# Kernel tuning notes

Measured on AMD Instinct MI355X. Metric: run time of the kernel, lower is better.

The kernel has to match this reference:

```python
import jax, jax.numpy as jnp
import numpy as np

B, N, C0, N0 = 2, 4096, 128, 10242
IN_CH = 19  # 16 class-label + 3 xyz channels of `original`
EPS = 1e-5


def setup_inputs() -> dict:
    key = jax.random.key(0)
    ks = jax.random.split(key, 8)
    original = jax.random.normal(ks[0], (B, IN_CH, N), dtype=jnp.float32)
    projected = jax.random.normal(ks[1], (B, C0, N0), dtype=jnp.float32)
    vertex = jax.random.normal(ks[2], (N0, 3), dtype=jnp.float32)
    near_idx = jax.random.randint(ks[3], (N0, 6), 1, N0)  # low=1 so threshold > 0
    W0 = jax.random.normal(ks[4], (128, IN_CH + C0), dtype=jnp.float32) * 0.02
    W1 = jax.random.normal(ks[5], (128, 128), dtype=jnp.float32) * 0.02
    W2 = jax.random.normal(ks[6], (128, 128), dtype=jnp.float32) * 0.02
    z = jnp.zeros((128,), jnp.float32)
    o = jnp.ones((128,), jnp.float32)
    return {
        'original': original, 'projected': projected, 'vertex': vertex,
        'near_idx': near_idx,
        'W0': W0, 'b0': z, 'g0': o, 'be0': z,
        'W1': W1, 'b1': z, 'g1': o, 'be1': z,
        'W2': W2, 'b2': z, 'g2': o, 'be2': z,
    }


def _sf_to_pc(proj_f, vertex, near_idx, xyz):
    # proj_f: [B, N0, C0] features per mesh vertex; xyz: [B, N, 3]
    r = jnp.sqrt(jnp.sum(vertex[0] ** 2))  # sphere radius of fractal mesh
    # spherical projection of xyz onto sphere radius r (same direction)
    pxyz = xyz * (r / jnp.linalg.norm(xyz, axis=-1, keepdims=True))  # [B,N,3]
    # threshold = dist(vertex[0], vertex[near_idx[0,0]]); compare squared dists
    t2 = jnp.sum((vertex[0] - vertex[near_idx[0, 0]]) ** 2)
    # squared distances via GEMM: |p|^2 = r^2 (on sphere)
    v2 = jnp.sum(vertex ** 2, axis=-1)  # [N0]
    d2 = r * r + v2[None, None, :] - 2.0 * jnp.einsum('bnd,md->bnm', pxyz, vertex)
    mask = d2 <= t2                              # [B,N,N0]
    has = jnp.any(mask, axis=-1)                 # [B,N]
    first = jnp.argmax(mask, axis=-1)            # first matching vertex (early-exit semantics)
    feat = jnp.take_along_axis(proj_f, first[..., None], axis=1)  # [B,N,C0]
    return jnp.where(has[..., None], feat, 0.0)


def _conv_bn_relu(x, W, b, g, be):
    # x: [B,N,Cin]; 1x1 Conv1d == per-point linear; BN over (B,N) per channel (train mode)
    y = jnp.einsum('bnc,oc->bno', x, W) + b
    mean = jnp.mean(y, axis=(0, 1))
    var = jnp.var(y, axis=(0, 1))
    y = g * (y - mean) * jax.lax.rsqrt(var + EPS) + be
    return jax.nn.relu(y)


def reference(original, projected, vertex, near_idx,
              W0, b0, g0, be0, W1, b1, g1, be1, W2, b2, g2, be2):
    orig = jnp.transpose(original, (0, 2, 1))    # [B,N,19]
    proj_f = jnp.transpose(projected, (0, 2, 1))  # [B,N0,C0]
    xyz = orig[:, :, :3]
    feat = _sf_to_pc(proj_f, vertex, near_idx, xyz)      # [B,N,C0]
    x = jnp.concatenate([orig, feat], axis=-1)           # [B,N,19+C0]
    x = _conv_bn_relu(x, W0, b0, g0, be0)
    x = _conv_bn_relu(x, W1, b1, g1, be1)
    x = _conv_bn_relu(x, W2, b2, g2, be2)
    return jnp.transpose(x, (0, 2, 1))  # [B,128,N]
```

## Files before the change

### kernel.cpp

```cpp
#include <hip/hip_runtime.h>

#define NPTS 4096
#define N0V  10242
#define EPSV 1e-5f
#define SLOTS 16

typedef unsigned short ushortT;
typedef __attribute__((ext_vector_type(8))) short short8;
typedef __attribute__((ext_vector_type(4))) float f32x4;

__device__ __forceinline__ float fmul(float a,float b){return __fmul_rn(a,b);}
__device__ __forceinline__ float fadd(float a,float b){return __fadd_rn(a,b);}
__device__ __forceinline__ float fsub(float a,float b){return __fsub_rn(a,b);}

__device__ __forceinline__ ushortT f2bf(float x){
  unsigned u = __float_as_uint(x);
  u = (u + 0x7fffu + ((u>>16)&1u)) >> 16;
  return (ushortT)u;
}
__device__ __forceinline__ float bf2f(ushortT u){
  return __uint_as_float(((unsigned)u) << 16);
}

template<int NS>
__device__ __forceinline__ void tile_mm(const ushortT* xa, const ushortT* wt, int wstr,
    int li, int hi, int rt, int colg, f32x4& acc)
{
  acc = (f32x4){0.f,0.f,0.f,0.f};
  const ushortT* wbp = wt + colg*wstr + hi*8;
  const ushortT* xap = xa + (rt*16 + li)*168 + hi*8;
  #pragma unroll
  for (int s=0;s<NS;s++){
    short8 bb = *(const short8*)(wbp + s*32);
    short8 a0 = *(const short8*)(xap + s*32);
    acc = __builtin_amdgcn_mfma_f32_16x16x32_bf16(a0, bb, acc, 0,0,0);
  }
}

__device__ __forceinline__ void tile_partials(const f32x4& acc, float* __restrict__ slotL,
                                              int blk, int lane, int colg)
{
  float s1=0.f, s2=0.f;
  #pragma unroll
  for (int r=0;r<4;r++){ s1 += acc[r]; s2 = fmaf(acc[r],acc[r],s2); }
  s1 += __shfl_xor(s1,16); s1 += __shfl_xor(s1,32);
  s2 += __shfl_xor(s2,16); s2 += __shfl_xor(s2,32);
  if (lane < 16){
    float* sl = slotL + (blk & (SLOTS-1))*256;
    atomicAdd(&sl[colg], s1);
    atomicAdd(&sl[128 + colg], s2);
  }
}

__device__ __forceinline__ void slot_stats(const float* __restrict__ slotL,
    const float* __restrict__ g, const float* __restrict__ be,
    float* red2, float* stS, float* stB, int t)
{
  if (t < 256){
    float v = 0.f;
    #pragma unroll
    for (int s=0;s<SLOTS;s++) v += slotL[s*256 + t];
    red2[t] = v;
  }
  __syncthreads();
  if (t < 128){
    float S = red2[t], Q = red2[128 + t];
    float mean = S * (1.0f/8192.0f);
    float var  = Q * (1.0f/8192.0f) - mean*mean;
    float inv  = 1.0f / __fsqrt_rn(var + EPSV);
    float sc = g[t]*inv;
    stS[t] = sc;
    stB[t] = be[t] - mean*sc;
  }
  __syncthreads();
}

__global__ __launch_bounds__(1024) void k_l0(
    const float* __restrict__ orig, const float* __restrict__ proj,
    const float* __restrict__ vertex, const int* __restrict__ nidx,
    const float* __restrict__ W0, const float* __restrict__ b0,
    float* __restrict__ slot0, float* __restrict__ slotZ,
    ushortT* __restrict__ y0)
{
  __shared__ __align__(16) ushortT wt[128*168];
  __shared__ __align__(16) ushortT xa[32*168];

  const int t    = threadIdx.x;
  const int blk  = blockIdx.x;
  const int lane = t & 63;
  const int w    = t >> 6;
  const int b    = blk >> 7;
  const int n0   = (blk & 127) * 32;
  const int li   = lane & 15;
  const int hi   = lane >> 4;
  const int rt   = w >> 3;
  const int colg = (w & 7)*16 + li;

  if (blk < 8) slotZ[blk*1024 + t] = 0.f;

  for (int u = t; u < 21504; u += 1024){
    int o = u/168, k = u - o*168;
    wt[u] = f2bf((k < 147) ? W0[o*147 + k] : 0.f);
  }

  {
    float v0x=vertex[0], v0y=vertex[1], v0z=vertex[2];
    float r  = __fsqrt_rn(fadd(fadd(fmul(v0x,v0x),fmul(v0y,v0y)),fmul(v0z,v0z)));
    float rr = fmul(r,r);
    int j0 = nidx[0];
    float ax=vertex[3*j0], ay=vertex[3*j0+1], az=vertex[3*j0+2];
    float dx=fsub(v0x,ax), dy=fsub(v0y,ay), dz=fsub(v0z,az);
    float t2 = fadd(fadd(fmul(dx,dx),fmul(dy,dy)),fmul(dz,dz));

    #pragma unroll
    for (int rr_i=0; rr_i<2; rr_i++){
      const int row = w*2 + rr_i;
      const int n = n0 + row;
      const float* ob = orig + (b*19)*NPTS + n;
      float x=ob[0], y=ob[NPTS], z=ob[2*NPTS];
      float nrm = __fsqrt_rn(fadd(fadd(fmul(x,x),fmul(y,y)),fmul(z,z)));
      float s = __fdiv_rn(r,nrm);
      float px=fmul(x,s), py=fmul(y,s), pz=fmul(z,s);

      int first=0, has=0;
      for (int c0=0; c0<N0V; c0+=256){
        int m0=min(c0+lane,N0V-1), m1=min(c0+lane+64,N0V-1),
            m2=min(c0+lane+128,N0V-1), m3=min(c0+lane+192,N0V-1);
        float a0x=vertex[3*m0],a0y=vertex[3*m0+1],a0z=vertex[3*m0+2];
        float a1x=vertex[3*m1],a1y=vertex[3*m1+1],a1z=vertex[3*m1+2];
        float a2x=vertex[3*m2],a2y=vertex[3*m2+1],a2z=vertex[3*m2+2];
        float a3x=vertex[3*m3],a3y=vertex[3*m3+1],a3z=vertex[3*m3+2];
        float v20=fadd(fadd(fmul(a0x,a0x),fmul(a0y,a0y)),fmul(a0z,a0z));
        float v21=fadd(fadd(fmul(a1x,a1x),fmul(a1y,a1y)),fmul(a1z,a1z));
        float v22=fadd(fadd(fmul(a2x,a2x),fmul(a2y,a2y)),fmul(a2z,a2z));
        float v23=fadd(fadd(fmul(a3x,a3x),fmul(a3y,a3y)),fmul(a3z,a3z));
        float d0=fadd(fadd(fmul(px,a0x),fmul(py,a0y)),fmul(pz,a0z));
        float d1=fadd(fadd(fmul(px,a1x),fmul(py,a1y)),fmul(pz,a1z));
        float d2=fadd(fadd(fmul(px,a2x),fmul(py,a2y)),fmul(pz,a2z));
        float d3=fadd(fadd(fmul(px,a3x),fmul(py,a3y)),fmul(pz,a3z));
        bool h0 = (c0+lane    <N0V) && (fsub(fadd(rr,v20),fmul(2.0f,d0)) <= t2);
        bool h1 = (c0+lane+64 <N0V) && (fsub(fadd(rr,v21),fmul(2.0f,d1)) <= t2);
        bool h2 = (c0+lane+128<N0V) && (fsub(fadd(rr,v22),fmul(2.0f,d2)) <= t2);
        bool h3 = (c0+lane+192<N0V) && (fsub(fadd(rr,v23),fmul(2.0f,d3)) <= t2);
        unsigned long long bal;
        if ((bal=__ballot(h0))){ first=c0     +__builtin_ctzll(bal); has=1; break; }
        if ((bal=__ballot(h1))){ first=c0+ 64+__builtin_ctzll(bal); has=1; break; }
        if ((bal=__ballot(h2))){ first=c0+128+__builtin_ctzll(bal); has=1; break; }
        if ((bal=__ballot(h3))){ first=c0+192+__builtin_ctzll(bal); has=1; break; }
      }

      ushortT* rowp = xa + row*168;
      const float* pb = proj + (long)b*128*N0V;
      #pragma unroll
      for (int k=0;k<3;k++){
        int idx = lane + k*64;
        if (idx < 168){
          float v;
          if (idx < 19)        v = orig[(b*19+idx)*NPTS + n];
          else if (idx < 147)  v = has ? pb[(long)(idx-19)*N0V + first] : 0.0f;
          else                 v = 0.0f;
          rowp[idx] = f2bf(v);
        }
      }
    }
  }
  __syncthreads();

  f32x4 acc;
  tile_mm<5>(xa, wt, 168, li, hi, rt, colg, acc);
  float bo = b0[colg];
  #pragma unroll
  for (int r=0;r<4;r++) acc[r] += bo;
  tile_partials(acc, slot0, blk, lane, colg);
  #pragma unroll
  for (int r=0;r<4;r++)
    y0[(long)(b*4096 + n0 + rt*16 + hi*4 + r)*128 + colg] = f2bf(acc[r]);
}

__global__ __launch_bounds__(1024) void k_lmid(
    const ushortT* __restrict__ yin, const float* __restrict__ slotPrev,
    const float* __restrict__ g, const float* __restrict__ be,
    const float* __restrict__ W, const float* __restrict__ bias,
    float* __restrict__ slotCur, ushortT* __restrict__ yout)
{
  __shared__ __align__(16) ushortT wt[128*136];
  __shared__ __align__(16) ushortT xa[32*168];
  __shared__ float red2[256];
  __shared__ float stS[128];
  __shared__ float stB[128];

  const int t    = threadIdx.x;
  const int blk  = blockIdx.x;
  const int lane = t & 63;
  const int w    = t >> 6;
  const int n0   = blk * 32;
  const int li   = lane & 15;
  const int hi   = lane >> 4;
  const int rt   = w >> 3;
  const int colg = (w & 7)*16 + li;

  for (int u = t; u < 17408; u += 1024){
    int o = u/136, k = u - o*136;
    wt[u] = f2bf((k < 128) ? W[o*128 + k] : 0.f);
  }
  for (int u = t; u < 1280; u += 1024){
    int row = u/40, c = 128 + (u - row*40);
    xa[row*168 + c] = 0;
  }
  slot_stats(slotPrev, g, be, red2, stS, stB, t);

  if (t < 512){
    int row = t >> 4, c0 = (t & 15) * 8;
    short8 yv = *(const short8*)(yin + (long)(n0+row)*128 + c0);
    short8 xv;
    #pragma unroll
    for (int j=0;j<8;j++){
      float f = bf2f((ushortT)yv[j]);
      f = fmaxf(fmaf(f, stS[c0+j], stB[c0+j]), 0.f);
      xv[j] = (short)f2bf(f);
    }
    *(short8*)(xa + row*168 + c0) = xv;
  }
  __syncthreads();

  f32x4 acc;
  tile_mm<4>(xa, wt, 136, li, hi, rt, colg, acc);
  float bo = bias[colg];
  #pragma unroll
  for (int r=0;r<4;r++) acc[r] += bo;
  tile_partials(acc, slotCur, blk, lane, colg);
  #pragma unroll
  for (int r=0;r<4;r++)
    yout[(long)(n0 + rt*16 + hi*4 + r)*128 + colg] = f2bf(acc[r]);
}

__global__ __launch_bounds__(1024) void k_out(
    const ushortT* __restrict__ yin, const float* __restrict__ slotPrev,
    const float* __restrict__ g, const float* __restrict__ be,
    float* __restrict__ out)
{
  __shared__ float ft[32*132];
  __shared__ float red2[256];
  __shared__ float stS[128];
  __shared__ float stB[128];

  const int t   = threadIdx.x;
  const int blk = blockIdx.x;
  const int b   = blk >> 7;
  const int n0  = (blk & 127) * 32;

  slot_stats(slotPrev, g, be, red2, stS, stB, t);

  if (t < 512){
    int row = t >> 4, c0 = (t & 15) * 8;
    short8 yv = *(const short8*)(yin + (long)(b*4096 + n0 + row)*128 + c0);
    #pragma unroll
    for (int j=0;j<8;j++)
      ft[row*132 + c0 + j] = fmaxf(fmaf(bf2f((ushortT)yv[j]), stS[c0+j], stB[c0+j]), 0.f);
  }
  __syncthreads();

  float* ob = out + (long)b*128*NPTS + n0;
  {
    int oo = t >> 3, jj = (t & 7) * 4;
    float4 v;
    v.x = ft[(jj  )*132 + oo];
    v.y = ft[(jj+1)*132 + oo];
    v.z = ft[(jj+2)*132 + oo];
    v.w = ft[(jj+3)*132 + oo];
    *(float4*)(ob + (long)oo*NPTS + jj) = v;
  }
}

extern "C" void kernel_launch(void* const* d_in, const int* in_sizes, int n_in,
                              void* d_out, int out_size, void* d_ws, size_t ws_size,
                              hipStream_t stream)
{
  const float* orig   = (const float*)d_in[0];
  const float* proj   = (const float*)d_in[1];
  const float* vertex = (const float*)d_in[2];
  const int*   nidx   = (const int*)d_in[3];
  const float* W0 = (const float*)d_in[4];
  const float* b0 = (const float*)d_in[5];
  const float* g0 = (const float*)d_in[6];
  const float* be0= (const float*)d_in[7];
  const float* W1 = (const float*)d_in[8];
  const float* b1 = (const float*)d_in[9];
  const float* g1 = (const float*)d_in[10];
  const float* be1= (const float*)d_in[11];
  const float* W2 = (const float*)d_in[12];
  const float* b2 = (const float*)d_in[13];
  const float* g2 = (const float*)d_in[14];
  const float* be2= (const float*)d_in[15];
  float* out = (float*)d_out;

  float*   ws    = (float*)d_ws;
  float*   slot0 = ws;
  float*   slot1 = ws + 4096;
  float*   slot2 = ws + 8192;
  ushortT* yA    = (ushortT*)(ws + 12288);
  ushortT* yB    = yA + 8192*128;

  hipMemsetAsync(d_ws, 0, 4096*sizeof(float), stream);

  k_l0  <<<256, 1024, 0, stream>>>(orig, proj, vertex, nidx, W0, b0, slot0, slot1, yA);
  k_lmid<<<256, 1024, 0, stream>>>(yA, slot0, g0, be0, W1, b1, slot1, yB);
  k_lmid<<<256, 1024, 0, stream>>>(yB, slot1, g1, be1, W2, b2, slot2, yA);
  k_out <<<256, 1024, 0, stream>>>(yA, slot2, g2, be2, out);
}
```

Baseline: 35.44 us.

## Fuse last conv layer with output via grid barrier; prepack bf16 weights

The third conv layer and the final BN+ReLU+transpose output kernel are merged into one cooperative kernel. It uses an atomic-counter grid barrier so that every block finishes its BN partials before the final statistics are read, and the layer-2 activations never go back to global memory. W1 and W2 are converted to bf16 once in the first kernel into a padded workspace package. Mid-layer kernels then copy that package into LDS with global_load_lds instead of converting fp32 weights in every block. The cost is a spin-wait barrier, which relies on all 256 blocks being co-resident, and some extra work in the first kernel.

```diff
diff --git a/kernel.cpp b/kernel.cpp
--- a/kernel.cpp
+++ b/kernel.cpp
@@ -3,6 +3,7 @@
 #define NPTS 4096
 #define N0V  10242
 #define EPSV 1e-5f
+#define NBLK 256
 #define SLOTS 16
 
 typedef unsigned short ushortT;
@@ -52,17 +53,10 @@
   }
 }
 
-__device__ __forceinline__ void slot_stats(const float* __restrict__ slotL,
+__device__ __forceinline__ void stats_from_red2(const float* red2,
     const float* __restrict__ g, const float* __restrict__ be,
-    float* red2, float* stS, float* stB, int t)
-{
-  if (t < 256){
-    float v = 0.f;
-    #pragma unroll
-    for (int s=0;s<SLOTS;s++) v += slotL[s*256 + t];
-    red2[t] = v;
-  }
-  __syncthreads();
+    float* stS, float* stB, int t)
+{
   if (t < 128){
     float S = red2[t], Q = red2[128 + t];
     float mean = S * (1.0f/8192.0f);
@@ -75,12 +69,39 @@
   __syncthreads();
 }
 
+__device__ __forceinline__ void slot_stats(const float* __restrict__ slotL,
+    const float* __restrict__ g, const float* __restrict__ be,
+    float* red2, float* stS, float* stB, int t)
+{
+  if (t < 256){
+    float v = 0.f;
+    #pragma unroll
+    for (int s=0;s<SLOTS;s++) v += slotL[s*256 + t];
+    red2[t] = v;
+  }
+  __syncthreads();
+  stats_from_red2(red2, g, be, stS, stB, t);
+}
+
+__device__ __forceinline__ void dma_w(const ushortT* __restrict__ src, ushortT* dst,
+                                      int nchunks, int w, int lane)
+{
+  const char* s = (const char*)src;
+  char* d = (char*)dst;
+  for (int i = w; i < nchunks; i += 16){
+    __builtin_amdgcn_global_load_lds(
+        (const __attribute__((address_space(1))) void*)(s + (size_t)i*1024 + (size_t)lane*16),
+        (__attribute__((address_space(3))) void*)(d + (size_t)i*1024), 16, 0, 0);
+  }
+}
+
 __global__ __launch_bounds__(1024) void k_l0(
     const float* __restrict__ orig, const float* __restrict__ proj,
     const float* __restrict__ vertex, const int* __restrict__ nidx,
     const float* __restrict__ W0, const float* __restrict__ b0,
+    const float* __restrict__ W1, const float* __restrict__ W2,
     float* __restrict__ slot0, float* __restrict__ slotZ,
-    ushortT* __restrict__ y0)
+    ushortT* __restrict__ wpkg, ushortT* __restrict__ y0)
 {
   __shared__ __align__(16) ushortT wt[128*168];
   __shared__ __align__(16) ushortT xa[32*168];
@@ -97,6 +118,15 @@
   const int colg = (w & 7)*16 + li;
 
   if (blk < 8) slotZ[blk*1024 + t] = 0.f;
+
+  if (t < 136){
+    int u = blk*136 + t;
+    int L = u / 17408, q = u - L*17408;
+    int o = q / 136, k = q - o*136;
+    float v = 0.f;
+    if (k < 128) v = (L == 0) ? W1[o*128 + k] : W2[o*128 + k];
+    wpkg[u] = f2bf(v);
+  }
 
   for (int u = t; u < 21504; u += 1024){
     int o = u/168, k = u - o*168;
@@ -180,7 +210,7 @@
 __global__ __launch_bounds__(1024) void k_lmid(
     const ushortT* __restrict__ yin, const float* __restrict__ slotPrev,
     const float* __restrict__ g, const float* __restrict__ be,
-    const float* __restrict__ W, const float* __restrict__ bias,
+    const ushortT* __restrict__ wpk, const float* __restrict__ bias,
     float* __restrict__ slotCur, ushortT* __restrict__ yout)
 {
   __shared__ __align__(16) ushortT wt[128*136];
@@ -199,10 +229,8 @@
   const int rt   = w >> 3;
   const int colg = (w & 7)*16 + li;
 
-  for (int u = t; u < 17408; u += 1024){
-    int o = u/136, k = u - o*136;
-    wt[u] = f2bf((k < 128) ? W[o*128 + k] : 0.f);
-  }
+  dma_w(wpk, wt, 34, w, lane);
+
   for (int u = t; u < 1280; u += 1024){
     int row = u/40, c = 128 + (u - row*40);
     xa[row*168 + c] = 0;
@@ -234,34 +262,91 @@
     yout[(long)(n0 + rt*16 + hi*4 + r)*128 + colg] = f2bf(acc[r]);
 }
 
-__global__ __launch_bounds__(1024) void k_out(
-    const ushortT* __restrict__ yin, const float* __restrict__ slotPrev,
-    const float* __restrict__ g, const float* __restrict__ be,
-    float* __restrict__ out)
-{
+struct FinParams {
+  const ushortT* yin; const float* slotPrev;
+  const float* g1; const float* be1;
+  const ushortT* wpk; const float* bias;
+  float* slotCur; int* cnt;
+  const float* g2; const float* be2;
+  float* out;
+};
+
+__global__ __launch_bounds__(1024) void k_final(FinParams p)
+{
+  __shared__ __align__(16) ushortT wt[128*136];
+  __shared__ __align__(16) ushortT xa[32*168];
   __shared__ float ft[32*132];
   __shared__ float red2[256];
   __shared__ float stS[128];
   __shared__ float stB[128];
 
-  const int t   = threadIdx.x;
-  const int blk = blockIdx.x;
-  const int b   = blk >> 7;
-  const int n0  = (blk & 127) * 32;
-
-  slot_stats(slotPrev, g, be, red2, stS, stB, t);
+  const int t    = threadIdx.x;
+  const int blk  = blockIdx.x;
+  const int lane = t & 63;
+  const int w    = t >> 6;
+  const int n0g  = blk * 32;
+  const int b    = blk >> 7;
+  const int n0   = (blk & 127) * 32;
+  const int li   = lane & 15;
+  const int hi   = lane >> 4;
+  const int rt   = w >> 3;
+  const int colg = (w & 7)*16 + li;
+
+  dma_w(p.wpk, wt, 34, w, lane);
+
+  for (int u = t; u < 1280; u += 1024){
+    int row = u/40, c = 128 + (u - row*40);
+    xa[row*168 + c] = 0;
+  }
+  slot_stats(p.slotPrev, p.g1, p.be1, red2, stS, stB, t);
 
   if (t < 512){
     int row = t >> 4, c0 = (t & 15) * 8;
-    short8 yv = *(const short8*)(yin + (long)(b*4096 + n0 + row)*128 + c0);
-    #pragma unroll
-    for (int j=0;j<8;j++)
-      ft[row*132 + c0 + j] = fmaxf(fmaf(bf2f((ushortT)yv[j]), stS[c0+j], stB[c0+j]), 0.f);
-  }
-  __syncthreads();
-
-  float* ob = out + (long)b*128*NPTS + n0;
+    short8 yv = *(const short8*)(p.yin + (long)(n0g+row)*128 + c0);
+    short8 xv;
+    #pragma unroll
+    for (int j=0;j<8;j++){
+      float f = bf2f((ushortT)yv[j]);
+      f = fmaxf(fmaf(f, stS[c0+j], stB[c0+j]), 0.f);
+      xv[j] = (short)f2bf(f);
+    }
+    *(short8*)(xa + row*168 + c0) = xv;
+  }
+  __syncthreads();
+
+  f32x4 acc;
+  tile_mm<4>(xa, wt, 136, li, hi, rt, colg, acc);
+  float bo = p.bias[colg];
+  #pragma unroll
+  for (int r=0;r<4;r++) acc[r] += bo;
+  tile_partials(acc, p.slotCur, blk, lane, colg);
+
+  __syncthreads();
+  if (t == 0){
+    __hip_atomic_fetch_add(p.cnt, 1, __ATOMIC_RELAXED, __HIP_MEMORY_SCOPE_AGENT);
+    while (__hip_atomic_load(p.cnt, __ATOMIC_RELAXED, __HIP_MEMORY_SCOPE_AGENT) < NBLK)
+      __builtin_amdgcn_s_sleep(1);
+  }
+  __syncthreads();
+  if (t < 256){
+    float v = 0.f;
+    #pragma unroll
+    for (int s=0;s<SLOTS;s++)
+      v += __hip_atomic_load(&p.slotCur[s*256 + t], __ATOMIC_RELAXED, __HIP_MEMORY_SCOPE_AGENT);
+    red2[t] = v;
+  }
+  __syncthreads();
+  stats_from_red2(red2, p.g2, p.be2, stS, stB, t);
+
   {
+    float ss = stS[colg], sb = stB[colg];
+    #pragma unroll
+    for (int r=0;r<4;r++)
+      ft[(rt*16 + hi*4 + r)*132 + colg] = fmaxf(fmaf(acc[r], ss, sb), 0.f);
+  }
+  __syncthreads();
+  {
+    float* ob = p.out + (long)b*128*NPTS + n0;
     int oo = t >> 3, jj = (t & 7) * 4;
     float4 v;
     v.x = ft[(jj  )*132 + oo];
@@ -296,15 +381,20 @@
 
   float*   ws    = (float*)d_ws;
   float*   slot0 = ws;
-  float*   slot1 = ws + 4096;
-  float*   slot2 = ws + 8192;
-  ushortT* yA    = (ushortT*)(ws + 12288);
+  int*     cnt   = (int*)(ws + 4096);
+  float*   slot1 = ws + 4112;
+  float*   slot2 = ws + 8208;
+  ushortT* wpkg  = (ushortT*)(ws + 12304);
+  ushortT* yA    = (ushortT*)(ws + 29712);
   ushortT* yB    = yA + 8192*128;
 
-  hipMemsetAsync(d_ws, 0, 4096*sizeof(float), stream);
-
-  k_l0  <<<256, 1024, 0, stream>>>(orig, proj, vertex, nidx, W0, b0, slot0, slot1, yA);
-  k_lmid<<<256, 1024, 0, stream>>>(yA, slot0, g0, be0, W1, b1, slot1, yB);
-  k_lmid<<<256, 1024, 0, stream>>>(yB, slot1, g1, be1, W2, b2, slot2, yA);
-  k_out <<<256, 1024, 0, stream>>>(yA, slot2, g2, be2, out);
-}
+  hipMemsetAsync(d_ws, 0, 4112*sizeof(float), stream);
+
+  k_l0  <<<256, 1024, 0, stream>>>(orig, proj, vertex, nidx, W0, b0, W1, W2,
+                                   slot0, slot1, wpkg, yA);
+  k_lmid<<<256, 1024, 0, stream>>>(yA, slot0, g0, be0, wpkg, b1, slot1, yB);
+
+  FinParams fp{yB, slot1, g1, be1, wpkg + 17408, b2, slot2, cnt, g2, be2, out};
+  void* args[] = {(void*)&fp};
+  hipLaunchCooperativeKernel((const void*)k_final, dim3(NBLK), dim3(1024), args, 0, stream);
+}
```

New measurement: 55.24 us. 1.56x slower.
